# Kernel optimization log

Hardware: AMD Instinct MI355X
Metric: run time of the kernel (lower is better)

## Reference

```python
import jax, jax.numpy as jnp
import numpy as np
import math

N, C, T, V = 8, 256, 128, 25
H, HC = 8, 32            # num_heads, head_channels
W, DIL = 3, 1            # window, dilation
O = 256                  # out_channels
PAD = (W + (W - 1) * (DIL - 1) - 1) // 2
B, L = N * T, W * V


def _ln(x, g, b):
    m = jnp.mean(x, -1, keepdims=True)
    v = jnp.var(x, -1, keepdims=True)
    return (x - m) * jax.lax.rsqrt(v + 1e-5) * g + b


def setup_inputs() -> dict:
    key = jax.random.key(0)
    ks = iter(jax.random.split(key, 40))
    def w(shape):
        return jax.random.normal(next(ks), shape, jnp.float32) * 0.02
    d = {"x": jax.random.normal(next(ks), (N, C, T, V), jnp.float32)}
    d.update(
        ln1_g=jnp.ones((C,)), ln1_b=jnp.zeros((C,)),
        Wq=w((C, C)), bq=jnp.zeros((C,)), Wqa=w((C, H)), bqa=jnp.zeros((H,)),
        Wk=w((C, C)), bk=jnp.zeros((C,)), Wka=w((C, H)), bka=jnp.zeros((H,)),
        Wv=w((C, C)), bv=jnp.zeros((C,)), Wt=w((C, C)), bt=jnp.zeros((C,)),
        Wp=w((C, C)), bp=jnp.zeros((C,)),
        ffn_g=jnp.ones((C,)), ffn_b=jnp.zeros((C,)),
        W1=w((C, C)), b1=jnp.zeros((C,)), W2=w((C, C)), b2=jnp.zeros((C,)),
        tn_g=jnp.ones((C,)), tn_b=jnp.zeros((C,)),
        c1_w=w((C, O)), c1_b=jnp.zeros((O,)),
        c2_w=w((W, O, O)), c2_b=jnp.zeros((O,)),
    )
    return d


def reference(x, ln1_g, ln1_b, Wq, bq, Wqa, bqa, Wk, bk, Wka, bka, Wv, bv,
              Wt, bt, Wp, bp, ffn_g, ffn_b, W1, b1, W2, b2, tn_g, tn_b,
              c1_w, c1_b, c2_w, c2_b):
    scale = 1.0 / math.sqrt(HC)
    # ---- Unfold over time: build window of frames around each t (nn.Unfold) ----
    xp = jnp.pad(x, ((0, 0), (0, 0), (PAD, PAD), (0, 0)))
    win = jnp.stack([jax.lax.dynamic_slice_in_dim(xp, k * DIL, T, 2) for k in range(W)], 2)  # (N,C,W,T,V)
    seq = win.transpose(0, 3, 2, 4, 1).reshape(B, L, C)  # (N*T, W*V, C)

    sep = lambda z: z.reshape(B, L, H, HC).transpose(0, 2, 1, 3)  # (B,H,L,HC)
    grp = lambda z: z.transpose(0, 2, 1, 3).reshape(B, -1, C)

    # ---- SpatioTemporalAttention (eval: dropouts off) ----
    nx = _ln(seq, ln1_g, ln1_b)
    q = nx @ Wq + bq                                            # (B,L,C)
    qw = jax.nn.softmax((q @ Wqa + bqa).transpose(0, 2, 1) * scale, axis=-1)  # (B,H,L)
    pq = jnp.einsum('bhl,bhlc->bhc', qw, sep(q)).reshape(B, 1, C)             # pooled query
    keys = nx @ Wk + bk
    kw = jax.nn.softmax(((keys * pq) @ Wka + bka).transpose(0, 2, 1) * scale, axis=-1)
    pk = jnp.einsum('bhl,bhlc->bhc', kw, sep(keys))             # pooled key (B,H,HC)
    vals = sep(nx @ Wv + bv)
    kv = grp(vals * pk[:, :, None, :]) @ Wt + bt                # (B,L,C)
    attn = (kv + q) @ Wp + bp                                   # residual-in-heads == plain add

    # ---- AttentionBranch residual + FFN ----
    att = attn + seq
    f = _ln(att, ffn_g, ffn_b)
    y = jax.nn.gelu(f @ W1 + b1, approximate=False) @ W2 + b2 + att  # (B,L,C)

    # ---- temporal branch: LN -> regroup frames -> 1x1 conv -> GELU -> (W,1) conv stride W ----
    t5 = _ln(y, tn_g, tn_b).reshape(N, T, W, V, C)
    h = jax.nn.gelu(t5 @ c1_w + c1_b, approximate=False)        # (N,T,W,V,O)
    out = jnp.einsum('ntwvi,wio->ntvo', h, c2_w) + c2_b         # stride==kernel conv == window contraction
    return out.transpose(0, 3, 1, 2)                            # (N,O,T,V)
```

## Files before the change

### kernel.cpp

```cpp
#include <hip/hip_runtime.h>


#define DI __device__ __forceinline__

constexpr int CC   = 256;
constexpr int CL   = 75;
constexpr int CV   = 25;
constexpr int CT   = 128;
constexpr int TP   = 130;
constexpr int MPAD = 8 * TP * CV;
constexpr int MBL  = 1024 * CL;
constexpr int MOUT = 8 * CT * CV;
constexpr float SM_SCALE = 0.17677669529663687f;

typedef __bf16 bf16x8 __attribute__((ext_vector_type(8)));
typedef float f32x4 __attribute__((ext_vector_type(4)));

DI float bf2f(unsigned short u) { return __uint_as_float(((unsigned)u) << 16); }
DI float bf2f_lo(unsigned u) { return __uint_as_float(u << 16); }
DI float bf2f_hi(unsigned u) { return __uint_as_float(u & 0xffff0000u); }
DI unsigned short f2bf(float f) {
  unsigned u = __float_as_uint(f);
  u += 0x7fffu + ((u >> 16) & 1u);
  return (unsigned short)(u >> 16);
}
DI unsigned packbf(float a, float b) {
  return (unsigned)f2bf(a) | ((unsigned)f2bf(b) << 16);
}
DI float geluf(float x) { return 0.5f * x * (1.f + erff(x * 0.70710678118654752440f)); }

DI void gll16(const unsigned short* g, unsigned short* l) {
  __builtin_amdgcn_global_load_lds(
      (const __attribute__((address_space(1))) unsigned int*)g,
      (__attribute__((address_space(3))) unsigned int*)l, 16, 0, 0);
}

DI int arow(int r) {
  int b = r / CL;
  int l = r - b * CL;
  int w = l / CV;
  int v = l - w * CV;
  int t = b & (CT - 1);
  int n = b >> 7;
  return (n * TP + t + w) * CV + v;
}

__global__ __launch_bounds__(256) void k_transpose(const float* __restrict__ x,
                                                   unsigned short* __restrict__ xtp) {
  __shared__ float tile[32][33];
  const int n = blockIdx.z;
  const int c0 = blockIdx.x * 32;
  const int tv0 = blockIdx.y * 32;
  const int tx = threadIdx.x & 31, ty = threadIdx.x >> 5;
#pragma unroll
  for (int j = 0; j < 32; j += 8) {
    tile[ty + j][tx] = x[((size_t)(n * CC + c0 + ty + j)) * 3200 + tv0 + tx];
  }
  __syncthreads();
#pragma unroll
  for (int j = 0; j < 32; j += 8) {
    int tv = tv0 + ty + j;
    int st = tv / CV, v = tv - st * CV;
    size_t row = ((size_t)n * TP + st + 1) * CV + v;
    xtp[row * CC + c0 + tx] = f2bf(tile[tx][ty + j]);
  }
}

__global__ __launch_bounds__(256) void k_zero_pad(unsigned short* __restrict__ xtp) {
  int i = blockIdx.x * 256 + threadIdx.x;
  int c = i & 255;
  int rid = i >> 8;
  int n = rid / 50;
  int rem = rid - n * 50;
  int side = rem / 25;
  int v = rem - side * 25;
  size_t row = ((size_t)n * TP + side * (TP - 1)) * CV + v;
  xtp[row * CC + c] = 0;
}

struct TJobs {
  const float* src[9];
  unsigned short* dst[9];
  int stride[9];
  int off[9];
};
__global__ __launch_bounds__(256) void k_wtrans(TJobs J) {
  __shared__ float tile[32][33];
  const int j = blockIdx.z;
  const float* src = J.src[j];
  unsigned short* dst = J.dst[j];
  const int stride = J.stride[j], off = J.off[j];
  const int k0 = blockIdx.x * 32, n0 = blockIdx.y * 32;
  const int tx = threadIdx.x & 31, ty = threadIdx.x >> 5;
#pragma unroll
  for (int jj = 0; jj < 32; jj += 8)
    tile[ty + jj][tx] = src[(size_t)(k0 + ty + jj) * 256 + n0 + tx];
  __syncthreads();
#pragma unroll
  for (int jj = 0; jj < 32; jj += 8)
    dst[(size_t)(n0 + ty + jj) * stride + off + k0 + tx] = f2bf(tile[tx][ty + jj]);
}

__global__ __launch_bounds__(256) void k_wtwp(const float* __restrict__ Wt,
                                              const float* __restrict__ Wq,
                                              const float* __restrict__ Wp,
                                              unsigned short* __restrict__ fusedB,
                                              unsigned short* __restrict__ WqWpT) {
  __shared__ float wrow[256];
  const int k = blockIdx.x, n = threadIdx.x;
  const float* src = blockIdx.y ? Wq : Wt;
  unsigned short* dst = blockIdx.y ? WqWpT : fusedB;
  wrow[n] = src[(size_t)k * 256 + n];
  __syncthreads();
  float acc = 0.f;
  for (int j = 0; j < 256; ++j) acc = fmaf(wrow[j], Wp[(size_t)j * 256 + n], acc);
  dst[(size_t)n * 256 + k] = f2bf(acc);
}

__global__ __launch_bounds__(256) void k_bias2(const float* __restrict__ bt,
                                               const float* __restrict__ Wp,
                                               const float* __restrict__ bp,
                                               const float* __restrict__ bq,
                                               const float* __restrict__ bk,
                                               const float* __restrict__ bv,
                                               float* __restrict__ bias2,
                                               float* __restrict__ bias3) {
  const int n = threadIdx.x;
  float acc = bp[n];
  float accq = 0.f;
  for (int j = 0; j < 256; ++j) {
    const float w = Wp[(size_t)j * 256 + n];
    acc = fmaf(bt[j], w, acc);
    accq = fmaf(bq[j], w, accq);
  }
  bias2[n] = acc;
  bias3[n] = bq[n];
  bias3[256 + n] = bk[n];
  bias3[512 + n] = bv[n];
  bias3[768 + n] = accq;
}

__global__ __launch_bounds__(256) void k_ln4(const unsigned short* __restrict__ X,
                                             const float* __restrict__ g,
                                             const float* __restrict__ b,
                                             unsigned short* __restrict__ Y) {
  const int row = blockIdx.x * 4 + (threadIdx.x >> 6);
  const int lane = threadIdx.x & 63;
  const uint2 u = *(const uint2*)(X + (size_t)row * CC + lane * 4);
  const float x0 = bf2f_lo(u.x), x1 = bf2f_hi(u.x), x2 = bf2f_lo(u.y), x3 = bf2f_hi(u.y);
  float s = x0 + x1 + x2 + x3;
  float q = x0 * x0 + x1 * x1 + x2 * x2 + x3 * x3;
#pragma unroll
  for (int o = 32; o; o >>= 1) { s += __shfl_xor(s, o); q += __shfl_xor(q, o); }
  const float mean = s * (1.f / CC);
  const float var = q * (1.f / CC) - mean * mean;
  const float rs = rsqrtf(var + 1e-5f);
  const float4 g4 = *(const float4*)(g + lane * 4);
  const float4 b4 = *(const float4*)(b + lane * 4);
  uint2 o2;
  o2.x = packbf((x0 - mean) * rs * g4.x + b4.x, (x1 - mean) * rs * g4.y + b4.y);
  o2.y = packbf((x2 - mean) * rs * g4.z + b4.z, (x3 - mean) * rs * g4.w + b4.w);
  *(uint2*)(Y + (size_t)row * CC + lane * 4) = o2;
}

template <int AMODE, int EPI, int KD, bool MULTI>
__global__ __launch_bounds__(512) void k_mgemm(const unsigned short* __restrict__ A,
                                               const unsigned short* __restrict__ BwT,
                                               const float* __restrict__ bias,
                                               unsigned short* __restrict__ Cout,
                                               float* __restrict__ FOut,
                                               int M) {
  if constexpr (MULTI) {
    const int z = blockIdx.y;
    BwT += (size_t)z * (256 * 256);
    bias += z * 256;
    Cout += (size_t)z * MPAD * CC;
  }
  __shared__ unsigned short SH[20480];
  const int tid = threadIdx.x;
  const int lane = tid & 63;
  const int wid = tid >> 6;
  const int wm = wid >> 2, wn = wid & 3;
  const int r0 = blockIdx.x * 64;
  f32x4 acc[2][4] = {};

  const bool sa = tid < 256;
  const int rA = r0 + (tid >> 2);
  const int rAc = (rA < M) ? rA : (M - 1);
  const int segs = ((tid & 3) ^ ((tid >> 3) & 3)) * 8;
  int hrb = 0;
  if (sa && AMODE == 4 && rA < M) {
    const int nb = rA / 3200, rr = rA - nb * 3200;
    const int tq = rr / 25, vq = rr - tq * 25;
    hrb = (nb * CT + tq) * CL + vq;
  }

  auto loadA4 = [&](int k0) -> uint4 {
    uint4 u = make_uint4(0, 0, 0, 0);
    if (!(sa && rA < M)) return u;
    const int w = k0 >> 8;
    u = *(const uint4*)(A + (size_t)(hrb + w * CV) * CC + (k0 & 255) + segs);
    return u;
  };
  auto stageB = [&](int buf, int k0) {
    unsigned short* bs = SH + 4096 + buf * 8192;
#pragma unroll
    for (int pp = 0; pp < 2; ++pp) {
      const int s = tid + pp * 512;
      const int cs = ((s & 3) ^ ((s >> 3) & 3)) * 8;
      gll16(BwT + (size_t)(s >> 2) * KD + k0 + cs, bs + s * 8);
    }
  };
  auto stageAg = [&](int buf, int k0) {
    if (sa) gll16(A + (size_t)rAc * CC + k0 + segs, SH + buf * 2048 + tid * 8);
  };
  const int swl = ((lane & 15) >> 1) & 3;
  auto mfmaStep = [&](int cur) {
    const unsigned short* as = SH + cur * 2048;
    const unsigned short* bs = SH + 4096 + cur * 8192;
    bf16x8 af[2], bfr[4];
#pragma unroll
    for (int mi = 0; mi < 2; ++mi)
      af[mi] = *(const bf16x8*)(as + (wm * 32 + mi * 16 + (lane & 15)) * 32 +
                                (((lane >> 4) ^ swl) * 8));
#pragma unroll
    for (int ni = 0; ni < 4; ++ni)
      bfr[ni] = *(const bf16x8*)(bs + (wn * 64 + ni * 16 + (lane & 15)) * 32 +
                                 (((lane >> 4) ^ swl) * 8));
#pragma unroll
    for (int mi = 0; mi < 2; ++mi)
#pragma unroll
      for (int ni = 0; ni < 4; ++ni)
        acc[mi][ni] = __builtin_amdgcn_mfma_f32_16x16x32_bf16(af[mi], bfr[ni], acc[mi][ni], 0, 0, 0);
  };

  constexpr int NT = KD / 32;
  if constexpr (AMODE == 0) {
    asm volatile("s_waitcnt vmcnt(0)" ::: "memory");
    stageB(0, 0);
    stageAg(0, 0);
    for (int t = 0; t < NT; ++t) {
      const int cur = t & 1;
      const bool more = (t + 1 < NT);
      if (more) { stageB(cur ^ 1, (t + 1) * 32); stageAg(cur ^ 1, (t + 1) * 32); }
      if (wid < 4) {
        if (more) asm volatile("s_waitcnt vmcnt(3)" ::: "memory");
        else      asm volatile("s_waitcnt vmcnt(0)" ::: "memory");
      } else {
        if (more) asm volatile("s_waitcnt vmcnt(2)" ::: "memory");
        else      asm volatile("s_waitcnt vmcnt(0)" ::: "memory");
      }
      __builtin_amdgcn_s_barrier();
      asm volatile("" ::: "memory");
      mfmaStep(cur);
      asm volatile("s_waitcnt lgkmcnt(0)" ::: "memory");
      __builtin_amdgcn_s_barrier();
      asm volatile("" ::: "memory");
    }
    __syncthreads();
  } else {
    {
      const uint4 a0 = loadA4(0);
      stageB(0, 0);
      if (sa) *(uint4*)(SH + tid * 8) = a0;
    }
    for (int t = 0; t < NT; ++t) {
      const int cur = t & 1;
      const bool more = (t + 1 < NT);
      if (more) {
        const uint4 an = loadA4((t + 1) * 32);
        stageB(cur ^ 1, (t + 1) * 32);
        if (sa) *(uint4*)(SH + (cur ^ 1) * 2048 + tid * 8) = an;
      }
      asm volatile("s_waitcnt lgkmcnt(0)" ::: "memory");
      if (more) asm volatile("s_waitcnt vmcnt(2)" ::: "memory");
      else      asm volatile("s_waitcnt vmcnt(0)" ::: "memory");
      __builtin_amdgcn_s_barrier();
      asm volatile("" ::: "memory");
      mfmaStep(cur);
      asm volatile("s_waitcnt lgkmcnt(0)" ::: "memory");
      __builtin_amdgcn_s_barrier();
      asm volatile("" ::: "memory");
    }
    if constexpr (EPI == 0) __syncthreads();
  }

  const int ln15 = lane & 15, lq = lane >> 4;
  if constexpr (EPI == 4) {
#pragma unroll
    for (int mi = 0; mi < 2; ++mi) {
#pragma unroll
      for (int ni = 0; ni < 4; ++ni) {
        const int col = wn * 64 + ni * 16 + ln15;
        const float bcol = bias[col];
        const int rbase = r0 + wm * 32 + mi * 16 + lq * 4;
        const int nb = rbase / 3200, rr = rbase - nb * 3200;
        float4 v;
        v.x = acc[mi][ni][0] + bcol;
        v.y = acc[mi][ni][1] + bcol;
        v.z = acc[mi][ni][2] + bcol;
        v.w = acc[mi][ni][3] + bcol;
        *(float4*)(FOut + (size_t)nb * 819200 + (size_t)col * 3200 + rr) = v;
      }
    }
  } else {
    constexpr int LDC = 260;
#pragma unroll
    for (int mi = 0; mi < 2; ++mi) {
#pragma unroll
      for (int ni = 0; ni < 4; ++ni) {
        const int col = wn * 64 + ni * 16 + ln15;
        const float bcol = bias[col];
#pragma unroll
        for (int rg = 0; rg < 4; ++rg) {
          const int lrow = wm * 32 + mi * 16 + lq * 4 + rg;
          SH[lrow * LDC + col] = f2bf(acc[mi][ni][rg] + bcol);
        }
      }
    }
    __syncthreads();
#pragma unroll
    for (int i = 0; i < 4; ++i) {
      const int idx = tid + i * 512;
      const int row = idx >> 5, ch = idx & 31;
      const int gr = r0 + row;
      if (gr < M)
        *(uint4*)(Cout + (size_t)gr * CC + ch * 8) = *(const uint4*)&SH[row * LDC + ch * 8];
    }
  }
}

__global__ __launch_bounds__(512, 4) void k_chain(
    const unsigned short* __restrict__ VP, const float* __restrict__ PK,
    const unsigned short* __restrict__ XTP, const unsigned short* __restrict__ QWPP,
    const unsigned short* __restrict__ fusedB, const float* __restrict__ bias2,
    const unsigned short* __restrict__ W1T, const float* __restrict__ b1,
    const unsigned short* __restrict__ W2T, const float* __restrict__ b2,
    const float* __restrict__ ffn_g, const float* __restrict__ ffn_b,
    const unsigned short* __restrict__ c1wT, const float* __restrict__ c1b,
    const float* __restrict__ tn_g, const float* __restrict__ tn_b,
    unsigned short* __restrict__ Hout) {
  constexpr int LDC = 264;
  __shared__ unsigned short SH[16896 + 4096 + 16384];
  unsigned short* ACT = SH;
  unsigned short* AS = SH + 16896;
  unsigned short* BS = SH + 16896 + 4096;
  const int tid = threadIdx.x;
  const int lane = tid & 63, wid = tid >> 6;
  const int wm = wid >> 2, wn = wid & 3;
  const int ln15 = lane & 15, lq = lane >> 4;
  const int swl = (ln15 >> 1) & 3;
  const int r0 = blockIdx.x * 64;

  const bool sa = tid < 256;
  const int rA = r0 + (tid >> 2);
  const int segs = ((tid & 3) ^ ((tid >> 3) & 3)) * 8;
  int ar = 0, bb = 0;
  if (sa) { ar = arow(rA); bb = rA / CL; }
  int xrow[8];
#pragma unroll
  for (int i = 0; i < 8; ++i)
    xrow[i] = arow(r0 + wm * 32 + (i >> 2) * 16 + lq * 4 + (i & 3));

  auto stageB = [&](const unsigned short* BwT, int KD, int buf, int k0) {
    unsigned short* bs = BS + buf * 8192;
#pragma unroll
    for (int pp = 0; pp < 2; ++pp) {
      const int s = tid + pp * 512;
      const int cs = ((s & 3) ^ ((s >> 3) & 3)) * 8;
      gll16(BwT + (size_t)(s >> 2) * KD + k0 + cs, bs + s * 8);
    }
  };
  auto loadA5 = [&](int k0) -> uint4 {
    uint4 u = make_uint4(0, 0, 0, 0);
    if (!sa) return u;
    const int kg = k0 + segs;
    const uint4 t4 = *(const uint4*)(VP + (size_t)ar * CC + kg);
    const float* sv = PK + bb * CC + kg;
    const float4 s0 = *(const float4*)sv;
    const float4 s1 = *(const float4*)(sv + 4);
    u.x = packbf(bf2f_lo(t4.x) * s0.x, bf2f_hi(t4.x) * s0.y);
    u.y = packbf(bf2f_lo(t4.y) * s0.z, bf2f_hi(t4.y) * s0.w);
    u.z = packbf(bf2f_lo(t4.z) * s1.x, bf2f_hi(t4.z) * s1.y);
    u.w = packbf(bf2f_lo(t4.w) * s1.z, bf2f_hi(t4.w) * s1.w);
    return u;
  };
  auto ln_inplace = [&](const float* g, const float* b) {
    const float4 g4 = *(const float4*)(g + lane * 4);
    const float4 b4 = *(const float4*)(b + lane * 4);
#pragma unroll
    for (int rr = 0; rr < 8; ++rr) {
      const int row = wid * 8 + rr;
      const uint2 u = *(const uint2*)(ACT + row * LDC + lane * 4);
      const float x0 = bf2f_lo(u.x), x1 = bf2f_hi(u.x);
      const float x2 = bf2f_lo(u.y), x3 = bf2f_hi(u.y);
      float s = x0 + x1 + x2 + x3;
      float q = x0 * x0 + x1 * x1 + x2 * x2 + x3 * x3;
#pragma unroll
      for (int o = 32; o; o >>= 1) { s += __shfl_xor(s, o); q += __shfl_xor(q, o); }
      const float mean = s * (1.f / CC);
      const float var = q * (1.f / CC) - mean * mean;
      const float rs = rsqrtf(var + 1e-5f);
      uint2 o2;
      o2.x = packbf((x0 - mean) * rs * g4.x + b4.x, (x1 - mean) * rs * g4.y + b4.y);
      o2.y = packbf((x2 - mean) * rs * g4.z + b4.z, (x3 - mean) * rs * g4.w + b4.w);
      *(uint2*)(ACT + row * LDC + lane * 4) = o2;
    }
  };
  auto gemmACT = [&](const unsigned short* BwT, f32x4 (&a)[2][4], bool prestaged) {
    if (!prestaged) {
      asm volatile("s_waitcnt vmcnt(0)" ::: "memory");
      stageB(BwT, 256, 0, 0);
    }
    for (int t = 0; t < 8; ++t) {
      const int cur = t & 1;
      const bool more = (t + 1 < 8);
      if (more) stageB(BwT, 256, cur ^ 1, (t + 1) * 32);
      bf16x8 af[2];
#pragma unroll
      for (int mi = 0; mi < 2; ++mi)
        af[mi] = *(const bf16x8*)(ACT + (wm * 32 + mi * 16 + ln15) * LDC + t * 32 + lq * 8);
      if (more) asm volatile("s_waitcnt vmcnt(2)" ::: "memory");
      else      asm volatile("s_waitcnt vmcnt(0)" ::: "memory");
      __builtin_amdgcn_s_barrier();
      asm volatile("" ::: "memory");
      bf16x8 bfr[4];
#pragma unroll
      for (int ni = 0; ni < 4; ++ni)
        bfr[ni] = *(const bf16x8*)(BS + cur * 8192 + (wn * 64 + ni * 16 + ln15) * 32 +
                                   ((lq ^ swl) * 8));
#pragma unroll
      for (int mi = 0; mi < 2; ++mi)
#pragma unroll
        for (int ni = 0; ni < 4; ++ni)
          a[mi][ni] = __builtin_amdgcn_mfma_f32_16x16x32_bf16(af[mi], bfr[ni], a[mi][ni], 0, 0, 0);
      asm volatile("s_waitcnt lgkmcnt(0)" ::: "memory");
      __builtin_amdgcn_s_barrier();
      asm volatile("" ::: "memory");
    }
  };

  f32x4 acc[2][4] = {};
  {
    const uint4 a0 = loadA5(0);
    stageB(fusedB, 256, 0, 0);
    if (sa) *(uint4*)(AS + tid * 8) = a0;
  }
  for (int t = 0; t < 8; ++t) {
    const int cur = t & 1;
    const bool more = (t + 1 < 8);
    if (more) {
      const uint4 an = loadA5((t + 1) * 32);
      stageB(fusedB, 256, cur ^ 1, (t + 1) * 32);
      if (sa) *(uint4*)(AS + (cur ^ 1) * 2048 + tid * 8) = an;
    }
    asm volatile("s_waitcnt lgkmcnt(0)" ::: "memory");
    if (more) asm volatile("s_waitcnt vmcnt(2)" ::: "memory");
    else      asm volatile("s_waitcnt vmcnt(0)" ::: "memory");
    __builtin_amdgcn_s_barrier();
    asm volatile("" ::: "memory");
    {
      bf16x8 af[2], bfr[4];
#pragma unroll
      for (int mi = 0; mi < 2; ++mi)
        af[mi] = *(const bf16x8*)(AS + cur * 2048 + (wm * 32 + mi * 16 + ln15) * 32 +
                                  ((lq ^ swl) * 8));
#pragma unroll
      for (int ni = 0; ni < 4; ++ni)
        bfr[ni] = *(const bf16x8*)(BS + cur * 8192 + (wn * 64 + ni * 16 + ln15) * 32 +
                                   ((lq ^ swl) * 8));
#pragma unroll
      for (int mi = 0; mi < 2; ++mi)
#pragma unroll
        for (int ni = 0; ni < 4; ++ni)
          acc[mi][ni] = __builtin_amdgcn_mfma_f32_16x16x32_bf16(af[mi], bfr[ni], acc[mi][ni], 0, 0, 0);
    }
    asm volatile("s_waitcnt lgkmcnt(0)" ::: "memory");
    __builtin_amdgcn_s_barrier();
    asm volatile("" ::: "memory");
  }
  stageB(W1T, 256, 0, 0);
  f32x4 attres[2][4];
#pragma unroll
  for (int mi = 0; mi < 2; ++mi) {
#pragma unroll
    for (int ni = 0; ni < 4; ++ni) {
      const int col = wn * 64 + ni * 16 + ln15;
      const float bcol = bias2[col];
#pragma unroll
      for (int rg = 0; rg < 4; ++rg) {
        const size_t ro = (size_t)xrow[mi * 4 + rg] * CC + col;
        attres[mi][ni][rg] = acc[mi][ni][rg] + bcol + bf2f(QWPP[ro]) + bf2f(XTP[ro]);
        ACT[(wm * 32 + mi * 16 + lq * 4 + rg) * LDC + col] = f2bf(attres[mi][ni][rg]);
      }
    }
  }
  __syncthreads();
  ln_inplace(ffn_g, ffn_b);
  __syncthreads();

  f32x4 acc2[2][4] = {};
  gemmACT(W1T, acc2, true);
  stageB(W2T, 256, 0, 0);
  __syncthreads();
#pragma unroll
  for (int mi = 0; mi < 2; ++mi)
#pragma unroll
    for (int ni = 0; ni < 4; ++ni) {
      const int col = wn * 64 + ni * 16 + ln15;
      const float bcol = b1[col];
#pragma unroll
      for (int rg = 0; rg < 4; ++rg)
        ACT[(wm * 32 + mi * 16 + lq * 4 + rg) * LDC + col] = f2bf(geluf(acc2[mi][ni][rg] + bcol));
    }
  __syncthreads();

  f32x4 acc3[2][4] = {};
  gemmACT(W2T, acc3, true);
  stageB(c1wT, 256, 0, 0);
  __syncthreads();
#pragma unroll
  for (int mi = 0; mi < 2; ++mi)
#pragma unroll
    for (int ni = 0; ni < 4; ++ni) {
      const int col = wn * 64 + ni * 16 + ln15;
      const float bcol = b2[col];
#pragma unroll
      for (int rg = 0; rg < 4; ++rg)
        ACT[(wm * 32 + mi * 16 + lq * 4 + rg) * LDC + col] =
            f2bf(acc3[mi][ni][rg] + bcol + attres[mi][ni][rg]);
    }
  __syncthreads();
  ln_inplace(tn_g, tn_b);
  __syncthreads();

  f32x4 acc4[2][4] = {};
  gemmACT(c1wT, acc4, true);
  __syncthreads();
#pragma unroll
  for (int mi = 0; mi < 2; ++mi)
#pragma unroll
    for (int ni = 0; ni < 4; ++ni) {
      const int col = wn * 64 + ni * 16 + ln15;
      const float bcol = c1b[col];
#pragma unroll
      for (int rg = 0; rg < 4; ++rg)
        ACT[(wm * 32 + mi * 16 + lq * 4 + rg) * LDC + col] = f2bf(geluf(acc4[mi][ni][rg] + bcol));
    }
  __syncthreads();
#pragma unroll
  for (int i = 0; i < 4; ++i) {
    const int idx = tid + i * 512;
    const int row = idx >> 5, ch = idx & 31;
    *(uint4*)(Hout + (size_t)(r0 + row) * CC + ch * 8) = *(const uint4*)&ACT[row * LDC + ch * 8];
  }
}

__global__ __launch_bounds__(256) void k_attpool2(
    const unsigned short* __restrict__ QPr, const unsigned short* __restrict__ KPr,
    const float* __restrict__ Wqa, const float* __restrict__ bqa,
    const float* __restrict__ Wka, const float* __restrict__ bka,
    float* __restrict__ PK) {
  __shared__ unsigned short rows[CL * CC];
  __shared__ float uu[8 * 258];
  __shared__ float lg[8 * 76];
  __shared__ float inv8[8];
  __shared__ float pq[256];
  __shared__ int arl[CL];
  const int b = blockIdx.x;
  const int t = threadIdx.x;

  if (t < CL) arl[t] = arow(b * CL + t);
  __syncthreads();

  auto dot_phase = [&](const float* b8) {
    const int c0 = (t & 63) * 4;
    for (int i = t; i < CL * 8; i += 256) {
      const int h = i / CL, l = i - h * CL;
      float acc = b8[h];
#pragma unroll 4
      for (int jj = 0; jj < CC; jj += 4) {
        const int c = (c0 + jj) & 255;
        const uint2 pr = *(const uint2*)&rows[l * CC + c];
        acc = fmaf(bf2f_lo(pr.x), uu[h * 258 + c], acc);
        acc = fmaf(bf2f_hi(pr.x), uu[h * 258 + c + 1], acc);
        acc = fmaf(bf2f_lo(pr.y), uu[h * 258 + c + 2], acc);
        acc = fmaf(bf2f_hi(pr.y), uu[h * 258 + c + 3], acc);
      }
      lg[h * 76 + l] = acc * SM_SCALE;
    }
  };
  auto softmax8 = [&]() {
    if (t < 8) {
      float m = -1e30f;
      for (int l = 0; l < CL; ++l) m = fmaxf(m, lg[t * 76 + l]);
      float s = 0.f;
      for (int l = 0; l < CL; ++l) {
        const float e = __expf(lg[t * 76 + l] - m);
        lg[t * 76 + l] = e;
        s += e;
      }
      inv8[t] = 1.f / s;
    }
  };

  for (int i = t; i < CL * 32; i += 256) {
    const int r = i >> 5, seg = i & 31;
    gll16(QPr + (size_t)arl[r] * CC + seg * 8, &rows[i * 8]);
  }
  for (int i = t; i < CC * 8; i += 256) {
    const int c = i >> 3, h = i & 7;
    uu[h * 258 + c] = Wqa[c * 8 + h];
  }
  __syncthreads();
  dot_phase(bqa);
  __syncthreads();
  softmax8();
  __syncthreads();
  {
    const int h = t >> 5;
    float acc = 0.f;
    for (int l = 0; l < CL; ++l) acc = fmaf(lg[h * 76 + l], bf2f(rows[l * CC + t]), acc);
    pq[t] = acc * inv8[h];
  }
  __syncthreads();

  for (int i = t; i < CL * 32; i += 256) {
    const int r = i >> 5, seg = i & 31;
    gll16(KPr + (size_t)arl[r] * CC + seg * 8, &rows[i * 8]);
  }
  for (int i = t; i < CC * 8; i += 256) {
    const int c = i >> 3, h = i & 7;
    uu[h * 258 + c] = pq[c] * Wka[c * 8 + h];
  }
  __syncthreads();
  dot_phase(bka);
  __syncthreads();
  softmax8();
  __syncthreads();
  {
    const int h = t >> 5;
    float acc = 0.f;
    for (int l = 0; l < CL; ++l) acc = fmaf(lg[h * 76 + l], bf2f(rows[l * CC + t]), acc);
    PK[(size_t)b * CC + t] = acc * inv8[h];
  }
}

extern "C" void kernel_launch(void* const* d_in, const int* in_sizes, int n_in,
                              void* d_out, int out_size, void* d_ws, size_t ws_size,
                              hipStream_t stream) {
  const float* x = (const float*)d_in[0];
  const float* ln1_g = (const float*)d_in[1];
  const float* ln1_b = (const float*)d_in[2];
  const float* Wq = (const float*)d_in[3];
  const float* bq = (const float*)d_in[4];
  const float* Wqa = (const float*)d_in[5];
  const float* bqa = (const float*)d_in[6];
  const float* Wk = (const float*)d_in[7];
  const float* bk = (const float*)d_in[8];
  const float* Wka = (const float*)d_in[9];
  const float* bka = (const float*)d_in[10];
  const float* Wv = (const float*)d_in[11];
  const float* bv = (const float*)d_in[12];
  const float* Wt = (const float*)d_in[13];
  const float* bt = (const float*)d_in[14];
  const float* Wp = (const float*)d_in[15];
  const float* bp = (const float*)d_in[16];
  const float* ffn_g = (const float*)d_in[17];
  const float* ffn_b = (const float*)d_in[18];
  const float* W1 = (const float*)d_in[19];
  const float* b1 = (const float*)d_in[20];
  const float* W2 = (const float*)d_in[21];
  const float* b2 = (const float*)d_in[22];
  const float* tn_g = (const float*)d_in[23];
  const float* tn_b = (const float*)d_in[24];
  const float* c1w = (const float*)d_in[25];
  const float* c1b = (const float*)d_in[26];
  const float* c2w = (const float*)d_in[27];
  const float* c2b = (const float*)d_in[28];
  float* out = (float*)d_out;

  char* wp = (char*)d_ws;
  auto alloc = [&](size_t bytes) -> char* {
    char* p = wp;
    wp += (bytes + 255) & ~(size_t)255;
    return p;
  };
  unsigned short* XTP = (unsigned short*)alloc((size_t)MPAD * CC * 2);
  unsigned short* LNXP = (unsigned short*)alloc((size_t)MPAD * CC * 2);
  unsigned short* QKVP = (unsigned short*)alloc((size_t)4 * MPAD * CC * 2);
  unsigned short* QP = QKVP;
  unsigned short* KP = QKVP + (size_t)MPAD * CC;
  unsigned short* VP = QKVP + (size_t)2 * MPAD * CC;
  unsigned short* QWPP = QKVP + (size_t)3 * MPAD * CC;
  unsigned short* Hb = (unsigned short*)alloc((size_t)MBL * CC * 2);
  float* PK = (float*)alloc((size_t)1024 * CC * 4);
  unsigned short* WqkvT = (unsigned short*)alloc((size_t)4 * 256 * 256 * 2);
  unsigned short* W1T = (unsigned short*)alloc(256 * 256 * 2);
  unsigned short* W2T = (unsigned short*)alloc(256 * 256 * 2);
  unsigned short* c1wT = (unsigned short*)alloc(256 * 256 * 2);
  unsigned short* c2wT = (unsigned short*)alloc(256 * 768 * 2);
  unsigned short* fusedB = (unsigned short*)alloc(256 * 256 * 2);
  float* bias2 = (float*)alloc(256 * 4);
  float* bias3 = (float*)alloc(1024 * 4);

  TJobs J;
  const float* srcs[9] = {Wq, Wk, Wv, W1, W2, c1w, c2w, c2w + 65536, c2w + 131072};
  unsigned short* dsts[9] = {WqkvT, WqkvT + 65536, WqkvT + 131072, W1T, W2T, c1wT,
                             c2wT, c2wT, c2wT};
  const int strides[9] = {256, 256, 256, 256, 256, 256, 768, 768, 768};
  const int offs[9] = {0, 0, 0, 0, 0, 0, 0, 256, 512};
  for (int i = 0; i < 9; ++i) {
    J.src[i] = srcs[i]; J.dst[i] = dsts[i]; J.stride[i] = strides[i]; J.off[i] = offs[i];
  }
  k_wtrans<<<dim3(8, 8, 9), 256, 0, stream>>>(J);
  k_wtwp<<<dim3(256, 2), 256, 0, stream>>>(Wt, Wq, Wp, fusedB, WqkvT + 3 * 65536);
  k_bias2<<<1, 256, 0, stream>>>(bt, Wp, bp, bq, bk, bv, bias2, bias3);

  k_transpose<<<dim3(8, 100, 8), 256, 0, stream>>>(x, XTP);
  k_zero_pad<<<400, 256, 0, stream>>>(XTP);
  k_ln4<<<MPAD / 4, 256, 0, stream>>>(XTP, ln1_g, ln1_b, LNXP);

  const int gP = (MPAD + 63) / 64;
  const int gO = MOUT / 64;
  k_mgemm<0, 0, 256, true><<<dim3(gP, 4), 512, 0, stream>>>(
      LNXP, WqkvT, bias3, QKVP, nullptr, MPAD);

  k_attpool2<<<1024, 256, 0, stream>>>(QP, KP, Wqa, bqa, Wka, bka, PK);

  k_chain<<<MBL / 64, 512, 0, stream>>>(VP, PK, XTP, QWPP, fusedB, bias2,
                                        W1T, b1, W2T, b2, ffn_g, ffn_b,
                                        c1wT, c1b, tn_g, tn_b, Hb);

  k_mgemm<4, 4, 768, false><<<gO, 512, 0, stream>>>(Hb, c2wT, c2b, nullptr, out, MOUT);
}
```

Measured before the change: 260.2 us.

## Load weight fragments directly from global into registers in chained GEMMs

Replaces the LDS-staged, barrier-synchronized B-operand pipeline in the three chained 256x256 GEMMs (W1, W2, c1) with per-wave register double-buffered loads straight from global memory. This removes two block barriers per k-step and the LDS staging traffic for weights. In exchange, every wave fetches its own B fragments through L1/L2 with no cross-wave sharing, and the loads are uncoalesced 16-byte row reads, so memory latency may be exposed.

```diff
diff --git a/kernel.cpp b/kernel.cpp
--- a/kernel.cpp
+++ b/kernel.cpp
@@ -407,36 +407,45 @@
       *(uint2*)(ACT + row * LDC + lane * 4) = o2;
     }
   };
-  auto gemmACT = [&](const unsigned short* BwT, f32x4 (&a)[2][4], bool prestaged) {
-    if (!prestaged) {
-      asm volatile("s_waitcnt vmcnt(0)" ::: "memory");
-      stageB(BwT, 256, 0, 0);
-    }
-    for (int t = 0; t < 8; ++t) {
-      const int cur = t & 1;
-      const bool more = (t + 1 < 8);
-      if (more) stageB(BwT, 256, cur ^ 1, (t + 1) * 32);
-      bf16x8 af[2];
-#pragma unroll
-      for (int mi = 0; mi < 2; ++mi)
-        af[mi] = *(const bf16x8*)(ACT + (wm * 32 + mi * 16 + ln15) * LDC + t * 32 + lq * 8);
-      if (more) asm volatile("s_waitcnt vmcnt(2)" ::: "memory");
-      else      asm volatile("s_waitcnt vmcnt(0)" ::: "memory");
-      __builtin_amdgcn_s_barrier();
-      asm volatile("" ::: "memory");
-      bf16x8 bfr[4];
+  auto gemmRB = [&](const unsigned short* BwT, f32x4 (&a)[2][4]) {
+    const unsigned short* bp = BwT + (size_t)(wn * 64 + ln15) * 256 + lq * 8;
+    const unsigned short* ap = ACT + (wm * 32 + ln15) * LDC + lq * 8;
+    bf16x8 bA[4], bB[4];
+#pragma unroll
+    for (int ni = 0; ni < 4; ++ni) bA[ni] = *(const bf16x8*)(bp + ni * 16 * 256);
+#pragma unroll 1
+    for (int tt = 0; tt < 4; ++tt) {
+      const int t0 = tt * 2, t1 = t0 + 1;
 #pragma unroll
       for (int ni = 0; ni < 4; ++ni)
-        bfr[ni] = *(const bf16x8*)(BS + cur * 8192 + (wn * 64 + ni * 16 + ln15) * 32 +
-                                   ((lq ^ swl) * 8));
-#pragma unroll
-      for (int mi = 0; mi < 2; ++mi)
+        bB[ni] = *(const bf16x8*)(bp + ni * 16 * 256 + t1 * 32);
+      {
+        bf16x8 af0[2];
+#pragma unroll
+        for (int mi = 0; mi < 2; ++mi)
+          af0[mi] = *(const bf16x8*)(ap + mi * 16 * LDC + t0 * 32);
+#pragma unroll
+        for (int mi = 0; mi < 2; ++mi)
+#pragma unroll
+          for (int ni = 0; ni < 4; ++ni)
+            a[mi][ni] = __builtin_amdgcn_mfma_f32_16x16x32_bf16(af0[mi], bA[ni], a[mi][ni], 0, 0, 0);
+      }
+      if (tt < 3) {
 #pragma unroll
         for (int ni = 0; ni < 4; ++ni)
-          a[mi][ni] = __builtin_amdgcn_mfma_f32_16x16x32_bf16(af[mi], bfr[ni], a[mi][ni], 0, 0, 0);
-      asm volatile("s_waitcnt lgkmcnt(0)" ::: "memory");
-      __builtin_amdgcn_s_barrier();
-      asm volatile("" ::: "memory");
+          bA[ni] = *(const bf16x8*)(bp + ni * 16 * 256 + (t0 + 2) * 32);
+      }
+      {
+        bf16x8 af1[2];
+#pragma unroll
+        for (int mi = 0; mi < 2; ++mi)
+          af1[mi] = *(const bf16x8*)(ap + mi * 16 * LDC + t1 * 32);
+#pragma unroll
+        for (int mi = 0; mi < 2; ++mi)
+#pragma unroll
+          for (int ni = 0; ni < 4; ++ni)
+            a[mi][ni] = __builtin_amdgcn_mfma_f32_16x16x32_bf16(af1[mi], bB[ni], a[mi][ni], 0, 0, 0);
+      }
     }
   };
 
@@ -479,7 +488,6 @@
     __builtin_amdgcn_s_barrier();
     asm volatile("" ::: "memory");
   }
-  stageB(W1T, 256, 0, 0);
   f32x4 attres[2][4];
 #pragma unroll
   for (int mi = 0; mi < 2; ++mi) {
@@ -500,8 +508,7 @@
   __syncthreads();
 
   f32x4 acc2[2][4] = {};
-  gemmACT(W1T, acc2, true);
-  stageB(W2T, 256, 0, 0);
+  gemmRB(W1T, acc2);
   __syncthreads();
 #pragma unroll
   for (int mi = 0; mi < 2; ++mi)
@@ -516,8 +523,7 @@
   __syncthreads();
 
   f32x4 acc3[2][4] = {};
-  gemmACT(W2T, acc3, true);
-  stageB(c1wT, 256, 0, 0);
+  gemmRB(W2T, acc3);
   __syncthreads();
 #pragma unroll
   for (int mi = 0; mi < 2; ++mi)
@@ -535,7 +541,7 @@
   __syncthreads();
 
   f32x4 acc4[2][4] = {};
-  gemmACT(c1wT, acc4, true);
+  gemmRB(c1wT, acc4);
   __syncthreads();
 #pragma unroll
   for (int mi = 0; mi < 2; ++mi)
```

Measured after the change: 321.0 us. 1.23x slower.
